# Kernel optimization log

Hardware: AMD Instinct MI355X
Metric: run time of the kernel (lower is better)

## Reference

```python
import jax, jax.numpy as jnp
import numpy as np

EPS = 1e-6
NEG = -10000.0  # matches _merge_attn_masks neg_inf

def rms(x, w):
    return x * jax.lax.rsqrt(jnp.mean(x * x, axis=-1, keepdims=True) + EPS) * w

def setup_inputs() -> dict:
    key = jax.random.key(0)
    ks = jax.random.split(key, 16)
    B, Tq, Tk, D, H, G, dh, F, E = 4, 1024, 1024, 1024, 16, 4, 64, 4096, 8
    s = 1.0 / np.sqrt(D)
    sf = 1.0 / np.sqrt(F)
    return {
        "x": jax.random.normal(ks[0], (B, Tq, D), jnp.float32),
        "k_ctx": jax.random.normal(ks[1], (B, Tk, G, dh), jnp.float32),
        "v_ctx": jax.random.normal(ks[2], (B, Tk, G, dh), jnp.float32),
        "sa_norm_w": jnp.ones((D,), jnp.float32),
        "w_qkv": jax.random.normal(ks[3], (D, 3 * D), jnp.float32) * s,
        "sa_wout": jax.random.normal(ks[4], (D, D), jnp.float32) * s,
        "ca_norm_w": jnp.ones((D,), jnp.float32),
        "w_q": jax.random.normal(ks[5], (D, D), jnp.float32) * s,
        "ca_wout": jax.random.normal(ks[6], (D, D), jnp.float32) * s,
        "moe_norm_w": jnp.ones((D,), jnp.float32),
        "w_gate": jax.random.normal(ks[7], (D, E), jnp.float32) * s,
        "w1": jax.random.normal(ks[8], (E, D, F), jnp.float32) * s,
        "b1": jnp.zeros((E, F), jnp.float32),
        "w2": jax.random.normal(ks[9], (E, F, D), jnp.float32) * sf,
        "b2": jnp.zeros((E, D), jnp.float32),
    }

def _attn(q, k, v, mask=None):
    # q,k,v: [B,H,T,dh]
    dh = q.shape[-1]
    scores = jnp.einsum("bhqd,bhkd->bhqk", q, k) / jnp.sqrt(jnp.float32(dh))
    if mask is not None:
        scores = scores + mask
    p = jax.nn.softmax(scores, axis=-1)
    return jnp.einsum("bhqk,bhkd->bhqd", p, v)

def reference(x, k_ctx, v_ctx, sa_norm_w, w_qkv, sa_wout, ca_norm_w, w_q, ca_wout,
              moe_norm_w, w_gate, w1, b1, w2, b2):
    B, Tq, D = x.shape
    Tk, G, dh = k_ctx.shape[1], k_ctx.shape[2], k_ctx.shape[3]
    H = 16
    rep = H // G

    # ---- self-attention (causal, pre-norm RMS, residual) ----
    xn = rms(x, sa_norm_w)
    qkv = xn @ w_qkv  # [B,Tq,3D]
    q, k, v = jnp.split(qkv, 3, axis=-1)
    split = lambda t: t.reshape(B, Tq, H, dh).transpose(0, 2, 1, 3)
    i = jnp.arange(Tq)[:, None]
    j = jnp.arange(Tq)[None, :]
    causal = jnp.where(j <= i, 0.0, NEG).astype(jnp.float32)[None, None]
    y = _attn(split(q), split(k), split(v), causal)
    y = y.transpose(0, 2, 1, 3).reshape(B, Tq, D) @ sa_wout
    x = x + y

    # ---- cross-attention GQA ----
    qc = rms(x, ca_norm_w) @ w_q
    qc = qc.reshape(B, Tq, H, dh).transpose(0, 2, 1, 3)
    kk = jnp.repeat(k_ctx, rep, axis=2).transpose(0, 2, 1, 3)  # [B,H,Tk,dh]
    vv = jnp.repeat(v_ctx, rep, axis=2).transpose(0, 2, 1, 3)
    yc = _attn(qc, kk, vv)
    yc = yc.transpose(0, 2, 1, 3).reshape(B, Tq, D) @ ca_wout
    x = x + yc

    # ---- top-1 MoE FFN ----
    xm = rms(x, moe_norm_w)
    gate_scores = jax.nn.softmax(xm @ w_gate, axis=-1)  # [B,T,E]
    top1_idx = jnp.argmax(gate_scores, axis=-1)
    top1_score = jnp.max(gate_scores, axis=-1)
    E = w1.shape[0]
    out = jnp.zeros_like(xm)
    for e in range(E):  # small fixed expert count
        ye = jax.nn.silu(xm @ w1[e] + b1[e]) @ w2[e] + b2[e]
        out = jnp.where((top1_idx == e)[..., None], ye, out)
    out = out * top1_score[..., None]
    return x + out
```

## Files before the change

### kernel.cpp

```cpp
#include <hip/hip_runtime.h>
#include <hip/hip_bf16.h>
#include <stdint.h>

#define B_  4
#define T_  1024
#define D_  1024
#define H_  16
#define DH  64
#define F_  4096
#define E_  8
#define NT  (B_*T_)

typedef float f32x4 __attribute__((ext_vector_type(4)));
typedef short bf16x8 __attribute__((ext_vector_type(8)));
#define MFMA_BF16 __builtin_amdgcn_mfma_f32_16x16x32_bf16

union PK8 { uint32_t u[4]; bf16x8 v; };

#define GL16(gsrc, ldst)                                                      \
  __builtin_amdgcn_global_load_lds(                                           \
      (const __attribute__((address_space(1))) void*)(const void*)(gsrc),     \
      (__attribute__((address_space(3))) void*)(void*)(ldst), 16, 0, 0)

static __device__ __forceinline__ uint16_t f2bf(float f) {
  uint32_t u = __float_as_uint(f);
  u += 0x7FFFu + ((u >> 16) & 1u);
  return (uint16_t)(u >> 16);
}
static __device__ __forceinline__ uint32_t packsplit(float f) {
  uint16_t h = f2bf(f);
  float hf = __uint_as_float(((uint32_t)h) << 16);
  uint16_t l = f2bf(f - hf);
  return ((uint32_t)h << 16) | (uint32_t)l;
}
static __device__ __forceinline__ void unpack8(const uint4 p0, const uint4 p1, bf16x8 &hi, bf16x8 &lo) {
  PK8 H, L;
  H.u[0] = __builtin_amdgcn_perm(p0.y, p0.x, 0x07060302u);
  L.u[0] = __builtin_amdgcn_perm(p0.y, p0.x, 0x05040100u);
  H.u[1] = __builtin_amdgcn_perm(p0.w, p0.z, 0x07060302u);
  L.u[1] = __builtin_amdgcn_perm(p0.w, p0.z, 0x05040100u);
  H.u[2] = __builtin_amdgcn_perm(p1.y, p1.x, 0x07060302u);
  L.u[2] = __builtin_amdgcn_perm(p1.y, p1.x, 0x05040100u);
  H.u[3] = __builtin_amdgcn_perm(p1.w, p1.z, 0x07060302u);
  L.u[3] = __builtin_amdgcn_perm(p1.w, p1.z, 0x05040100u);
  hi = H.v; lo = L.v;
}

__global__ __launch_bounds__(256) void k_pack_t2(const float* __restrict__ in,
                                                 uint16_t* __restrict__ outh, uint16_t* __restrict__ outl,
                                                 int K, int N) {
  __shared__ float t[32][33];
  const size_t mo = (size_t)blockIdx.z * K * N;
  in += mo; outh += mo; outl += mo;
  int n0 = blockIdx.x * 32, k0 = blockIdx.y * 32;
  int tx = threadIdx.x & 31, ty = threadIdx.x >> 5;
#pragma unroll
  for (int i = 0; i < 32; i += 8) t[ty + i][tx] = in[(size_t)(k0 + ty + i) * N + n0 + tx];
  __syncthreads();
#pragma unroll
  for (int i = 0; i < 32; i += 8) {
    float v = t[tx][ty + i];
    uint16_t h = f2bf(v);
    uint16_t l = f2bf(v - __uint_as_float((uint32_t)h << 16));
    size_t o = (size_t)(n0 + ty + i) * K + k0 + tx;
    outh[o] = h; outl[o] = l;
  }
}

__global__ __launch_bounds__(256) void k_bf_t(const float* __restrict__ in, uint16_t* __restrict__ out,
                                              int K, int N) {
  __shared__ float t[64][65];
  const size_t mo = (size_t)blockIdx.z * K * N;
  in += mo; out += mo;
  int n0 = blockIdx.x * 64, k0 = blockIdx.y * 64;
  int tr = threadIdx.x >> 4;
  int tc = (threadIdx.x & 15) * 4;
#pragma unroll
  for (int i = 0; i < 64; i += 16) {
    float4 v = *(const float4*)&in[(size_t)(k0 + tr + i) * N + n0 + tc];
    t[tr + i][tc] = v.x; t[tr + i][tc + 1] = v.y; t[tr + i][tc + 2] = v.z; t[tr + i][tc + 3] = v.w;
  }
  __syncthreads();
#pragma unroll
  for (int i = 0; i < 64; i += 16) {
    int n = tr + i;
    uint16_t b0 = f2bf(t[tc][n]), b1 = f2bf(t[tc + 1][n]);
    uint16_t b2 = f2bf(t[tc + 2][n]), b3 = f2bf(t[tc + 3][n]);
    uint2 wv;
    wv.x = ((uint32_t)b1 << 16) | b0;
    wv.y = ((uint32_t)b3 << 16) | b2;
    *(uint2*)&out[(size_t)(n0 + n) * K + k0 + tc] = wv;
  }
}

__global__ __launch_bounds__(256) void k_t32(const uint32_t* __restrict__ in, uint32_t* __restrict__ outp) {
  __shared__ uint32_t t[32][33];
  int b = blockIdx.z, t0 = blockIdx.x * 32, c0 = blockIdx.y * 32;
  int tx = threadIdx.x & 31, ty = threadIdx.x >> 5;
#pragma unroll
  for (int i = 0; i < 32; i += 8)
    t[ty + i][tx] = in[(size_t)(b * T_ + t0 + ty + i) * 3072 + 2048 + c0 + tx];
  __syncthreads();
#pragma unroll
  for (int i = 0; i < 32; i += 8)
    outp[(size_t)(b * T_ + c0 + ty + i) * T_ + t0 + tx] = t[tx][ty + i];
}

__global__ __launch_bounds__(256) void k_packf(const float* __restrict__ in, uint32_t* __restrict__ out) {
  int i = (blockIdx.x * 256 + threadIdx.x) * 4;
  float4 v = *(const float4*)&in[i];
  out[i] = packsplit(v.x); out[i+1] = packsplit(v.y); out[i+2] = packsplit(v.z); out[i+3] = packsplit(v.w);
}

__global__ __launch_bounds__(256) void k_tf32(const float* __restrict__ in, uint32_t* __restrict__ outp) {
  __shared__ float t[32][33];
  int b = blockIdx.z, t0 = blockIdx.x * 32, c0 = blockIdx.y * 32;
  int tx = threadIdx.x & 31, ty = threadIdx.x >> 5;
#pragma unroll
  for (int i = 0; i < 32; i += 8)
    t[ty + i][tx] = in[(size_t)(b * T_ + t0 + ty + i) * 256 + c0 + tx];
  __syncthreads();
#pragma unroll
  for (int i = 0; i < 32; i += 8)
    outp[(size_t)(b * 256 + c0 + ty + i) * T_ + t0 + tx] = packsplit(t[tx][ty + i]);
}

__global__ __launch_bounds__(256) void k_rms(const float* __restrict__ x, const float* __restrict__ w,
                                             uint16_t* __restrict__ oh, uint16_t* __restrict__ ol,
                                             const float* __restrict__ wg, int* __restrict__ idxp,
                                             float* __restrict__ scb) {
  int row = blockIdx.x;
  const float* xr = x + (size_t)row * D_;
  int t = threadIdx.x;
  float4 xv = *(const float4*)&xr[t * 4];
  float s = xv.x * xv.x + xv.y * xv.y + xv.z * xv.z + xv.w * xv.w;
#pragma unroll
  for (int o = 32; o; o >>= 1) s += __shfl_xor(s, o, 64);
  __shared__ float ps[4];
  __shared__ float ga[4][8];
  if ((t & 63) == 0) ps[t >> 6] = s;
  __syncthreads();
  s = ps[0] + ps[1] + ps[2] + ps[3];
  float sc = 1.0f / sqrtf(s * (1.0f / (float)D_) + 1e-6f);
  float4 wv = *(const float4*)&w[t * 4];
  float o0 = xv.x * sc * wv.x, o1 = xv.y * sc * wv.y, o2 = xv.z * sc * wv.z, o3 = xv.w * sc * wv.w;
  uint16_t h0 = f2bf(o0), h1 = f2bf(o1), h2 = f2bf(o2), h3 = f2bf(o3);
  if (oh) {
    uint2 ph;
    ph.x = ((uint32_t)h1 << 16) | h0;
    ph.y = ((uint32_t)h3 << 16) | h2;
    *(uint2*)&oh[(size_t)row * D_ + t * 4] = ph;
  }
  if (ol) {
    uint16_t l0 = f2bf(o0 - __uint_as_float((uint32_t)h0 << 16));
    uint16_t l1 = f2bf(o1 - __uint_as_float((uint32_t)h1 << 16));
    uint16_t l2 = f2bf(o2 - __uint_as_float((uint32_t)h2 << 16));
    uint16_t l3 = f2bf(o3 - __uint_as_float((uint32_t)h3 << 16));
    uint2 pl;
    pl.x = ((uint32_t)l1 << 16) | l0;
    pl.y = ((uint32_t)l3 << 16) | l2;
    *(uint2*)&ol[(size_t)row * D_ + t * 4] = pl;
  }
  if (wg) {
    float a[8] = {};
    float ov[4] = {o0, o1, o2, o3};
#pragma unroll
    for (int j = 0; j < 4; j++) {
      const float* wr = &wg[(size_t)(t * 4 + j) * 8];
      float4 wa = *(const float4*)wr, wb = *(const float4*)(wr + 4);
      float v = ov[j];
      a[0] += v * wa.x; a[1] += v * wa.y; a[2] += v * wa.z; a[3] += v * wa.w;
      a[4] += v * wb.x; a[5] += v * wb.y; a[6] += v * wb.z; a[7] += v * wb.w;
    }
#pragma unroll
    for (int e = 0; e < 8; e++)
#pragma unroll
      for (int o = 32; o; o >>= 1) a[e] += __shfl_xor(a[e], o, 64);
    if ((t & 63) == 0)
#pragma unroll
      for (int e = 0; e < 8; e++) ga[t >> 6][e] = a[e];
    __syncthreads();
    if (t == 0) {
      float g[8];
#pragma unroll
      for (int e = 0; e < 8; e++) g[e] = ga[0][e] + ga[1][e] + ga[2][e] + ga[3][e];
      int bi = 0; float bv = g[0];
#pragma unroll
      for (int e = 1; e < 8; e++) if (g[e] > bv) { bv = g[e]; bi = e; }
      float se = 0.f;
#pragma unroll
      for (int e = 0; e < 8; e++) se += expf(g[e] - bv);
      idxp[row] = bi;
      scb[row] = 1.0f / se;
    }
  }
}

#define GBM 128
#define GBN 64
__global__ __launch_bounds__(256) void k_gemm_split(const uint16_t* __restrict__ Ahg, const uint16_t* __restrict__ Alg,
                                                    const uint16_t* __restrict__ Whg, const uint16_t* __restrict__ Wlg,
                                                    float* __restrict__ C, const float* __restrict__ res,
                                                    uint32_t* __restrict__ Cpk, int scale_cols,
                                                    int M, int N, int K) {
  __shared__ uint16_t Ah[2][GBM][32], Al[2][GBM][32];
  __shared__ uint16_t Wh[2][GBN][32], Wl[2][GBN][32];
  int m0 = blockIdx.y * GBM, n0 = blockIdx.x * GBN;
  int tid = threadIdx.x, wv = tid >> 6, ln = tid & 63, mi = ln & 15, b8 = ln >> 4;
  int lr = ln >> 2, lc = ln & 3;
  int cg = lc ^ (lr & 3);
  int rowA = wv * 32 + lr;
  int rowW = wv * 16 + lr;
  const uint16_t* pAh  = Ahg + (size_t)(m0 + rowA) * K + cg * 8;
  const uint16_t* pAl  = Alg + (size_t)(m0 + rowA) * K + cg * 8;
  const uint16_t* pAh2 = pAh + (size_t)16 * K;
  const uint16_t* pAl2 = pAl + (size_t)16 * K;
  const uint16_t* pWh  = Whg + (size_t)(n0 + rowW) * K + cg * 8;
  const uint16_t* pWl  = Wlg + (size_t)(n0 + rowW) * K + cg * 8;
  const int ch8 = (b8 ^ (mi & 3)) * 8;
  f32x4 acc[2][4] = {};

#define STAGE(bf) do {                                                         \
    GL16(pAh,  &Ah[bf][wv * 32][0]);                                           \
    GL16(pAh2, &Ah[bf][wv * 32 + 16][0]);                                      \
    GL16(pAl,  &Al[bf][wv * 32][0]);                                           \
    GL16(pAl2, &Al[bf][wv * 32 + 16][0]);                                      \
    GL16(pWh,  &Wh[bf][wv * 16][0]);                                           \
    GL16(pWl,  &Wl[bf][wv * 16][0]);                                           \
    pAh += 32; pAh2 += 32; pAl += 32; pAl2 += 32; pWh += 32; pWl += 32;        \
  } while (0)

  const int NK = K >> 5;
  STAGE(0);
  __syncthreads();
  int cur = 0;
  for (int t = 0; t < NK; ++t) {
    if (t + 1 < NK) STAGE(cur ^ 1);
    bf16x8 ah[2], al[2], bh[4], bl[4];
#pragma unroll
    for (int fm = 0; fm < 2; fm++) {
      ah[fm] = *(const bf16x8*)&Ah[cur][wv * 32 + fm * 16 + mi][ch8];
      al[fm] = *(const bf16x8*)&Al[cur][wv * 32 + fm * 16 + mi][ch8];
    }
#pragma unroll
    for (int fn = 0; fn < 4; fn++) {
      bh[fn] = *(const bf16x8*)&Wh[cur][fn * 16 + mi][ch8];
      bl[fn] = *(const bf16x8*)&Wl[cur][fn * 16 + mi][ch8];
    }
#pragma unroll
    for (int fm = 0; fm < 2; fm++)
#pragma unroll
      for (int fn = 0; fn < 4; fn++) {
        acc[fm][fn] = MFMA_BF16(al[fm], bh[fn], acc[fm][fn], 0, 0, 0);
        acc[fm][fn] = MFMA_BF16(ah[fm], bl[fn], acc[fm][fn], 0, 0, 0);
        acc[fm][fn] = MFMA_BF16(ah[fm], bh[fn], acc[fm][fn], 0, 0, 0);
      }
    __syncthreads();
    cur ^= 1;
  }
#undef STAGE
#pragma unroll
  for (int fm = 0; fm < 2; fm++)
#pragma unroll
    for (int fn = 0; fn < 4; fn++)
#pragma unroll
      for (int rr = 0; rr < 4; rr++) {
        int row = m0 + wv * 32 + fm * 16 + b8 * 4 + rr;
        int col = n0 + fn * 16 + mi;
        float v = acc[fm][fn][rr];
        if (Cpk) {
          if (col < scale_cols) v *= 0.125f;
          Cpk[(size_t)row * N + col] = packsplit(v);
        } else {
          if (res) v += res[(size_t)row * N + col];
          C[(size_t)row * N + col] = v;
        }
      }
}

template <bool CAUSAL>
__global__ __launch_bounds__(256, 3) void k_fattn(
    const uint32_t* __restrict__ qp, int qs,
    const uint32_t* __restrict__ kp, int ks_, int khdiv,
    const uint32_t* __restrict__ vtp, int nvrows,
    uint16_t* __restrict__ yhg, uint16_t* __restrict__ ylg) {
  __shared__ uint32_t Ks[64][68];
  __shared__ uint32_t Vs[64][68];
  __shared__ uint32_t Ps[4][32][36];
  const int qt = blockIdx.x, h = blockIdx.y, b = blockIdx.z;
  const int tid = threadIdx.x, wv = tid >> 6, ln = tid & 63, mi = ln & 15, b8 = ln >> 4;
  const int koff = (h / khdiv) * 64;
  const uint32_t* kbase = kp + (size_t)b * T_ * ks_ + koff;
  const uint32_t* vbase = vtp + ((size_t)b * nvrows + koff) * T_;

  bf16x8 qh[2][2], ql[2][2];
#pragma unroll
  for (int u = 0; u < 2; u++)
#pragma unroll
    for (int k2 = 0; k2 < 2; k2++) {
      const uint32_t* p = qp + (size_t)(b * T_ + qt * 128 + wv * 32 + u * 16 + mi) * qs + h * 64 + k2 * 32 + b8 * 8;
      unpack8(*(const uint4*)p, *(const uint4*)(p + 4), qh[u][k2], ql[u][k2]);
    }

  float m[2][4], l[2][4];
  f32x4 o[2][4] = {};
#pragma unroll
  for (int u = 0; u < 2; u++)
#pragma unroll
    for (int r = 0; r < 4; r++) { m[u][r] = -1e30f; l[u][r] = 0.f; }

  const int nkt = CAUSAL ? (2 * qt + 2) : (T_ / 64);
  for (int kt = 0; kt < nkt; kt++) {
    __syncthreads();
    {
      int rr = tid >> 2, cc = (tid & 3) * 16;
      const uint32_t* src = kbase + (size_t)(kt * 64 + rr) * ks_ + cc;
      *(uint4*)&Ks[rr][cc]      = *(const uint4*)src;
      *(uint4*)&Ks[rr][cc + 4]  = *(const uint4*)(src + 4);
      *(uint4*)&Ks[rr][cc + 8]  = *(const uint4*)(src + 8);
      *(uint4*)&Ks[rr][cc + 12] = *(const uint4*)(src + 12);
      const uint32_t* vsrc = vbase + (size_t)rr * T_ + kt * 64 + cc;
      *(uint4*)&Vs[rr][cc]      = *(const uint4*)vsrc;
      *(uint4*)&Vs[rr][cc + 4]  = *(const uint4*)(vsrc + 4);
      *(uint4*)&Vs[rr][cc + 8]  = *(const uint4*)(vsrc + 8);
      *(uint4*)&Vs[rr][cc + 12] = *(const uint4*)(vsrc + 12);
    }
    __syncthreads();
#pragma unroll
    for (int s = 0; s < 2; s++) {
      bf16x8 kh[2][2], kl[2][2];
#pragma unroll
      for (int nf = 0; nf < 2; nf++)
#pragma unroll
        for (int k2 = 0; k2 < 2; k2++) {
          const uint32_t* p = &Ks[s * 32 + nf * 16 + mi][k2 * 32 + b8 * 8];
          unpack8(*(const uint4*)p, *(const uint4*)(p + 4), kh[nf][k2], kl[nf][k2]);
        }
      f32x4 a[2][2] = {};
#pragma unroll
      for (int u = 0; u < 2; u++)
#pragma unroll
        for (int nf = 0; nf < 2; nf++)
#pragma unroll
          for (int k2 = 0; k2 < 2; k2++) {
            a[u][nf] = MFMA_BF16(ql[u][k2], kh[nf][k2], a[u][nf], 0, 0, 0);
            a[u][nf] = MFMA_BF16(qh[u][k2], kl[nf][k2], a[u][nf], 0, 0, 0);
            a[u][nf] = MFMA_BF16(qh[u][k2], kh[nf][k2], a[u][nf], 0, 0, 0);
          }
      if (CAUSAL && kt >= 2 * qt) {
        int kg = kt * 64 + s * 32 + mi;
#pragma unroll
        for (int u = 0; u < 2; u++) {
          int qg = qt * 128 + wv * 32 + u * 16 + b8 * 4;
#pragma unroll
          for (int r = 0; r < 4; r++) {
            if (kg > qg + r)      a[u][0][r] = -1e30f;
            if (kg + 16 > qg + r) a[u][1][r] = -1e30f;
          }
        }
      }
#pragma unroll
      for (int u = 0; u < 2; u++) {
        float pm[4];
#pragma unroll
        for (int r = 0; r < 4; r++) pm[r] = fmaxf(a[u][0][r], a[u][1][r]);
#pragma unroll
        for (int off = 1; off <= 8; off <<= 1)
#pragma unroll
          for (int r = 0; r < 4; r++) pm[r] = fmaxf(pm[r], __shfl_xor(pm[r], off, 64));
        float sc[4];
#pragma unroll
        for (int r = 0; r < 4; r++) {
          float mn = fmaxf(m[u][r], pm[r]);
          sc[r] = __expf(m[u][r] - mn);
          m[u][r] = mn;
          a[u][0][r] = __expf(a[u][0][r] - mn);
          a[u][1][r] = __expf(a[u][1][r] - mn);
        }
        float rs[4];
#pragma unroll
        for (int r = 0; r < 4; r++) rs[r] = a[u][0][r] + a[u][1][r];
#pragma unroll
        for (int off = 1; off <= 8; off <<= 1)
#pragma unroll
          for (int r = 0; r < 4; r++) rs[r] += __shfl_xor(rs[r], off, 64);
#pragma unroll
        for (int r = 0; r < 4; r++) l[u][r] = l[u][r] * sc[r] + rs[r];
#pragma unroll
        for (int f = 0; f < 4; f++)
#pragma unroll
          for (int r = 0; r < 4; r++) o[u][f][r] *= sc[r];
#pragma unroll
        for (int r = 0; r < 4; r++) {
          uint32_t Hw, Lw;
          asm("v_cvt_pk_bf16_f32 %0, %1, %2" : "=v"(Hw) : "v"(a[u][0][r]), "v"(a[u][1][r]));
          float h0 = __uint_as_float(Hw << 16);
          float h1 = __uint_as_float(Hw & 0xffff0000u);
          float r0 = a[u][0][r] - h0, r1 = a[u][1][r] - h1;
          asm("v_cvt_pk_bf16_f32 %0, %1, %2" : "=v"(Lw) : "v"(r0), "v"(r1));
          Ps[wv][u * 16 + b8 * 4 + r][mi]      = __builtin_amdgcn_perm(Hw, Lw, 0x05040100u);
          Ps[wv][u * 16 + b8 * 4 + r][16 + mi] = __builtin_amdgcn_perm(Hw, Lw, 0x07060302u);
        }
      }
      bf16x8 ph[2], pl[2];
#pragma unroll
      for (int u = 0; u < 2; u++) {
        const uint32_t* p = &Ps[wv][u * 16 + mi][b8 * 8];
        unpack8(*(const uint4*)p, *(const uint4*)(p + 4), ph[u], pl[u]);
      }
#pragma unroll
      for (int f = 0; f < 4; f++) {
        bf16x8 vh, vl;
        const uint32_t* p = &Vs[f * 16 + mi][s * 32 + b8 * 8];
        unpack8(*(const uint4*)p, *(const uint4*)(p + 4), vh, vl);
#pragma unroll
        for (int u = 0; u < 2; u++) {
          o[u][f] = MFMA_BF16(pl[u], vh, o[u][f], 0, 0, 0);
          o[u][f] = MFMA_BF16(ph[u], vl, o[u][f], 0, 0, 0);
          o[u][f] = MFMA_BF16(ph[u], vh, o[u][f], 0, 0, 0);
        }
      }
    }
  }
#pragma unroll
  for (int u = 0; u < 2; u++)
#pragma unroll
    for (int r = 0; r < 4; r++) {
      float inv = 1.0f / l[u][r];
      int row = qt * 128 + wv * 32 + u * 16 + b8 * 4 + r;
#pragma unroll
      for (int f = 0; f < 4; f++) {
        size_t idx = (size_t)(b * T_ + row) * D_ + h * 64 + f * 16 + mi;
        float v = o[u][f][r] * inv;
        uint16_t hv = f2bf(v);
        yhg[idx] = hv;
        ylg[idx] = f2bf(v - __uint_as_float((uint32_t)hv << 16));
      }
    }
}

__global__ __launch_bounds__(256) void k_bucket(const int* __restrict__ idx, int* __restrict__ cnt,
                                                int* __restrict__ lists) {
  int tok = blockIdx.x * 256 + threadIdx.x;
  int e = idx[tok];
  int p = atomicAdd(&cnt[e], 1);
  lists[e * NT + p] = tok;
}

__global__ __launch_bounds__(256) void k_moe1(const uint16_t* __restrict__ xmbf, const uint16_t* __restrict__ w1t,
                                              const float* __restrict__ b1, const int* __restrict__ cnt,
                                              const int* __restrict__ lists, uint16_t* __restrict__ hbf) {
  int e = blockIdx.z;
  int c = cnt[e];
  int m0 = blockIdx.y * 64;
  if (m0 >= c) return;
  int n0 = blockIdx.x * 64;
  __shared__ uint16_t As[64][72];
  __shared__ uint16_t Ws[64][72];
  __shared__ int toks[64];
  int tid = threadIdx.x, wv = tid >> 6, ln = tid & 63, mi = ln & 15, b8 = ln >> 4;
  if (tid < 64) toks[tid] = (m0 + tid < c) ? lists[e * NT + m0 + tid] : -1;
  __syncthreads();
  int r = tid >> 2, c16 = (tid & 3) * 16;
  int tk = toks[r];
  const uint16_t* asrc = (tk >= 0) ? (xmbf + (size_t)tk * D_ + c16) : nullptr;
  const uint16_t* wsrc = w1t + (size_t)e * F_ * D_ + (size_t)(n0 + r) * D_ + c16;
  f32x4 acc[4] = {};
  for (int k0 = 0; k0 < D_; k0 += 64) {
    {
      uint4 a0 = make_uint4(0, 0, 0, 0), a1 = make_uint4(0, 0, 0, 0);
      if (asrc) { a0 = *(const uint4*)(asrc + k0); a1 = *(const uint4*)(asrc + k0 + 8); }
      uint4 w0 = *(const uint4*)(wsrc + k0), w1v = *(const uint4*)(wsrc + k0 + 8);
      *(uint4*)&As[r][c16] = a0; *(uint4*)&As[r][c16 + 8] = a1;
      *(uint4*)&Ws[r][c16] = w0; *(uint4*)&Ws[r][c16 + 8] = w1v;
    }
    __syncthreads();
#pragma unroll
    for (int ks = 0; ks < 2; ks++) {
      bf16x8 a = *(const bf16x8*)&As[wv * 16 + mi][ks * 32 + b8 * 8];
#pragma unroll
      for (int fn = 0; fn < 4; fn++) {
        bf16x8 bb = *(const bf16x8*)&Ws[fn * 16 + mi][ks * 32 + b8 * 8];
        acc[fn] = MFMA_BF16(a, bb, acc[fn], 0, 0, 0);
      }
    }
    __syncthreads();
  }
#pragma unroll
  for (int fn = 0; fn < 4; fn++)
#pragma unroll
    for (int rr = 0; rr < 4; rr++) {
      int rt = wv * 16 + b8 * 4 + rr;
      if (m0 + rt < c) {
        int tok = toks[rt];
        int col = n0 + fn * 16 + mi;
        float v = acc[fn][rr] + b1[e * F_ + col];
        v = v / (1.0f + expf(-v));
        hbf[(size_t)tok * F_ + col] = f2bf(v);
      }
    }
}

__global__ __launch_bounds__(256) void k_moe2(const uint16_t* __restrict__ hbf, const uint16_t* __restrict__ w2t,
                                              const float* __restrict__ b2, const float* __restrict__ x2,
                                              const float* __restrict__ sc, const int* __restrict__ cnt,
                                              const int* __restrict__ lists, float* __restrict__ out) {
  int e = blockIdx.z;
  int c = cnt[e];
  int m0 = blockIdx.y * 64;
  if (m0 >= c) return;
  int n0 = blockIdx.x * 64;
  __shared__ uint16_t As[64][72];
  __shared__ uint16_t Ws[64][72];
  __shared__ int toks[64];
  int tid = threadIdx.x, wv = tid >> 6, ln = tid & 63, mi = ln & 15, b8 = ln >> 4;
  if (tid < 64) toks[tid] = (m0 + tid < c) ? lists[e * NT + m0 + tid] : -1;
  __syncthreads();
  int r = tid >> 2, c16 = (tid & 3) * 16;
  int tk = toks[r];
  const uint16_t* asrc = (tk >= 0) ? (hbf + (size_t)tk * F_ + c16) : nullptr;
  const uint16_t* wsrc = w2t + (size_t)e * D_ * F_ + (size_t)(n0 + r) * F_ + c16;
  f32x4 acc[4] = {};
  for (int k0 = 0; k0 < F_; k0 += 64) {
    {
      uint4 a0 = make_uint4(0, 0, 0, 0), a1 = make_uint4(0, 0, 0, 0);
      if (asrc) { a0 = *(const uint4*)(asrc + k0); a1 = *(const uint4*)(asrc + k0 + 8); }
      uint4 w0 = *(const uint4*)(wsrc + k0), w1v = *(const uint4*)(wsrc + k0 + 8);
      *(uint4*)&As[r][c16] = a0; *(uint4*)&As[r][c16 + 8] = a1;
      *(uint4*)&Ws[r][c16] = w0; *(uint4*)&Ws[r][c16 + 8] = w1v;
    }
    __syncthreads();
#pragma unroll
    for (int ks = 0; ks < 2; ks++) {
      bf16x8 a = *(const bf16x8*)&As[wv * 16 + mi][ks * 32 + b8 * 8];
#pragma unroll
      for (int fn = 0; fn < 4; fn++) {
        bf16x8 bb = *(const bf16x8*)&Ws[fn * 16 + mi][ks * 32 + b8 * 8];
        acc[fn] = MFMA_BF16(a, bb, acc[fn], 0, 0, 0);
      }
    }
    __syncthreads();
  }
#pragma unroll
  for (int fn = 0; fn < 4; fn++)
#pragma unroll
    for (int rr = 0; rr < 4; rr++) {
      int rt = wv * 16 + b8 * 4 + rr;
      if (m0 + rt < c) {
        int tok = toks[rt];
        int col = n0 + fn * 16 + mi;
        float v = acc[fn][rr] + b2[e * D_ + col];
        out[(size_t)tok * D_ + col] = x2[(size_t)tok * D_ + col] + sc[tok] * v;
      }
    }
}

extern "C" void kernel_launch(void* const* d_in, const int* in_sizes, int n_in,
                              void* d_out, int out_size, void* d_ws, size_t ws_size,
                              hipStream_t stream) {
  const float* x       = (const float*)d_in[0];
  const float* k_ctx   = (const float*)d_in[1];
  const float* v_ctx   = (const float*)d_in[2];
  const float* sa_nw   = (const float*)d_in[3];
  const float* w_qkv   = (const float*)d_in[4];
  const float* sa_wout = (const float*)d_in[5];
  const float* ca_nw   = (const float*)d_in[6];
  const float* w_q     = (const float*)d_in[7];
  const float* ca_wout = (const float*)d_in[8];
  const float* moe_nw  = (const float*)d_in[9];
  const float* w_gate  = (const float*)d_in[10];
  const float* w1      = (const float*)d_in[11];
  const float* b1      = (const float*)d_in[12];
  const float* w2      = (const float*)d_in[13];
  const float* b2      = (const float*)d_in[14];
  float* out = (float*)d_out;
  (void)in_sizes; (void)n_in; (void)out_size; (void)ws_size;

  char* ws = (char*)d_ws;
  size_t off = 0;
  auto alloc = [&](size_t bytes) { char* p = ws + off; off += (bytes + 255) & ~(size_t)255; return p; };
  uint16_t* xnh   = (uint16_t*)alloc((size_t)NT * D_ * 2);
  uint16_t* xnl   = (uint16_t*)alloc((size_t)NT * D_ * 2);
  uint16_t* yh    = (uint16_t*)alloc((size_t)NT * D_ * 2);
  uint16_t* yl    = (uint16_t*)alloc((size_t)NT * D_ * 2);
  float*    x1    = (float*)alloc((size_t)NT * D_ * 4);
  uint32_t* qkv_pk = (uint32_t*)alloc((size_t)NT * 3 * D_ * 4);
  uint32_t* qc_pk = qkv_pk;
  float* x2 = (float*)(qkv_pk + (size_t)NT * D_);
  uint16_t* wqkvTh = (uint16_t*)alloc((size_t)D_ * 3 * D_ * 2);
  uint16_t* wqkvTl = (uint16_t*)alloc((size_t)D_ * 3 * D_ * 2);
  uint16_t* sawTh  = (uint16_t*)alloc((size_t)D_ * D_ * 2);
  uint16_t* sawTl  = (uint16_t*)alloc((size_t)D_ * D_ * 2);
  uint16_t* wqTh   = (uint16_t*)alloc((size_t)D_ * D_ * 2);
  uint16_t* wqTl   = (uint16_t*)alloc((size_t)D_ * D_ * 2);
  uint16_t* cawTh  = (uint16_t*)alloc((size_t)D_ * D_ * 2);
  uint16_t* cawTl  = (uint16_t*)alloc((size_t)D_ * D_ * 2);
  uint16_t* w1t   = (uint16_t*)alloc((size_t)E_ * D_ * F_ * 2);
  uint16_t* w2t   = (uint16_t*)alloc((size_t)E_ * D_ * F_ * 2);
  uint16_t* hbf   = (uint16_t*)alloc((size_t)NT * F_ * 2);
  uint32_t* vt    = (uint32_t*)hbf;
  uint32_t* kc_pk = (uint32_t*)((char*)hbf + (size_t)16 * 1024 * 1024);
  uint32_t* vct   = (uint32_t*)((char*)hbf + (size_t)20 * 1024 * 1024);
  uint16_t* xmbf  = (uint16_t*)alloc((size_t)NT * D_ * 2);
  int*   idx   = (int*)alloc(NT * 4);
  float* scb   = (float*)alloc(NT * 4);
  int*   cnt   = (int*)alloc(256);
  int*   lists = (int*)alloc((size_t)E_ * NT * 4);

  k_pack_t2<<<dim3(3 * D_ / 32, D_ / 32, 1), 256, 0, stream>>>(w_qkv, wqkvTh, wqkvTl, D_, 3 * D_);
  k_pack_t2<<<dim3(D_ / 32, D_ / 32, 1), 256, 0, stream>>>(sa_wout, sawTh, sawTl, D_, D_);
  k_pack_t2<<<dim3(D_ / 32, D_ / 32, 1), 256, 0, stream>>>(w_q, wqTh, wqTl, D_, D_);
  k_pack_t2<<<dim3(D_ / 32, D_ / 32, 1), 256, 0, stream>>>(ca_wout, cawTh, cawTl, D_, D_);
  k_bf_t<<<dim3(F_ / 64, D_ / 64, E_), 256, 0, stream>>>(w1, w1t, D_, F_);
  k_bf_t<<<dim3(D_ / 64, F_ / 64, E_), 256, 0, stream>>>(w2, w2t, F_, D_);
  k_packf<<<(B_ * T_ * 256) / 1024, 256, 0, stream>>>(k_ctx, kc_pk);
  k_tf32<<<dim3(T_ / 32, 256 / 32, B_), 256, 0, stream>>>(v_ctx, vct);

  k_rms<<<NT, 256, 0, stream>>>(x, sa_nw, xnh, xnl, nullptr, nullptr, nullptr);
  k_gemm_split<<<dim3(3 * D_ / GBN, NT / GBM), 256, 0, stream>>>(xnh, xnl, wqkvTh, wqkvTl, nullptr, nullptr, qkv_pk, 1024, NT, 3 * D_, D_);
  k_t32<<<dim3(T_ / 32, D_ / 32, B_), 256, 0, stream>>>(qkv_pk, vt);
  k_fattn<true><<<dim3(T_ / 128, H_, B_), 256, 0, stream>>>(qkv_pk, 3072, qkv_pk + 1024, 3072, 1, vt, 1024, yh, yl);
  k_gemm_split<<<dim3(D_ / GBN, NT / GBM), 256, 0, stream>>>(yh, yl, sawTh, sawTl, x1, x, nullptr, 0, NT, D_, D_);

  k_rms<<<NT, 256, 0, stream>>>(x1, ca_nw, xnh, xnl, nullptr, nullptr, nullptr);
  k_gemm_split<<<dim3(D_ / GBN, NT / GBM), 256, 0, stream>>>(xnh, xnl, wqTh, wqTl, nullptr, nullptr, qc_pk, 1024, NT, D_, D_);
  k_fattn<false><<<dim3(T_ / 128, H_, B_), 256, 0, stream>>>(qc_pk, 1024, kc_pk, 256, 4, vct, 256, yh, yl);
  k_gemm_split<<<dim3(D_ / GBN, NT / GBM), 256, 0, stream>>>(yh, yl, cawTh, cawTl, x2, x1, nullptr, 0, NT, D_, D_);

  k_rms<<<NT, 256, 0, stream>>>(x2, moe_nw, xmbf, nullptr, w_gate, idx, scb);
  hipMemsetAsync(cnt, 0, 32, stream);
  k_bucket<<<NT / 256, 256, 0, stream>>>(idx, cnt, lists);
  k_moe1<<<dim3(F_ / 64, NT / 64, E_), 256, 0, stream>>>(xmbf, w1t, b1, cnt, lists, hbf);
  k_moe2<<<dim3(D_ / 64, NT / 64, E_), 256, 0, stream>>>(hbf, w2t, b2, x2, scb, cnt, lists, out);
}
```

Before: 852.4 us.

## Store attention operands as separate bf16 hi/lo planes instead of packed words

```diff
diff --git a/kernel.cpp b/kernel.cpp
--- a/kernel.cpp
+++ b/kernel.cpp
@@ -26,12 +26,6 @@
   uint32_t u = __float_as_uint(f);
   u += 0x7FFFu + ((u >> 16) & 1u);
   return (uint16_t)(u >> 16);
-}
-static __device__ __forceinline__ uint32_t packsplit(float f) {
-  uint16_t h = f2bf(f);
-  float hf = __uint_as_float(((uint32_t)h) << 16);
-  uint16_t l = f2bf(f - hf);
-  return ((uint32_t)h << 16) | (uint32_t)l;
 }
 static __device__ __forceinline__ void unpack8(const uint4 p0, const uint4 p1, bf16x8 &hi, bf16x8 &lo) {
   PK8 H, L;
@@ -93,26 +87,51 @@
   }
 }
 
-__global__ __launch_bounds__(256) void k_t32(const uint32_t* __restrict__ in, uint32_t* __restrict__ outp) {
-  __shared__ uint32_t t[32][33];
-  int b = blockIdx.z, t0 = blockIdx.x * 32, c0 = blockIdx.y * 32;
-  int tx = threadIdx.x & 31, ty = threadIdx.x >> 5;
-#pragma unroll
-  for (int i = 0; i < 32; i += 8)
-    t[ty + i][tx] = in[(size_t)(b * T_ + t0 + ty + i) * 3072 + 2048 + c0 + tx];
-  __syncthreads();
-#pragma unroll
-  for (int i = 0; i < 32; i += 8)
-    outp[(size_t)(b * T_ + c0 + ty + i) * T_ + t0 + tx] = t[tx][ty + i];
-}
-
-__global__ __launch_bounds__(256) void k_packf(const float* __restrict__ in, uint32_t* __restrict__ out) {
+__global__ __launch_bounds__(256) void k_t16(const uint16_t* __restrict__ inh, const uint16_t* __restrict__ inl,
+                                             uint16_t* __restrict__ outh, uint16_t* __restrict__ outl) {
+  __shared__ uint16_t th[64][68], tl[64][68];
+  int b = blockIdx.z, t0 = blockIdx.x * 64, c0 = blockIdx.y * 64;
+  int tr = threadIdx.x >> 4;
+  int tc = (threadIdx.x & 15) * 4;
+#pragma unroll
+  for (int i = 0; i < 64; i += 16) {
+    size_t src = (size_t)(b * T_ + t0 + tr + i) * 3072 + 2048 + c0 + tc;
+    *(uint2*)&th[tr + i][tc] = *(const uint2*)&inh[src];
+    *(uint2*)&tl[tr + i][tc] = *(const uint2*)&inl[src];
+  }
+  __syncthreads();
+#pragma unroll
+  for (int i = 0; i < 64; i += 16) {
+    int n = tr + i;
+    size_t dst = (size_t)(b * 1024 + c0 + n) * T_ + t0 + tc;
+    uint2 ph, pl;
+    ph.x = ((uint32_t)th[tc + 1][n] << 16) | th[tc][n];
+    ph.y = ((uint32_t)th[tc + 3][n] << 16) | th[tc + 2][n];
+    pl.x = ((uint32_t)tl[tc + 1][n] << 16) | tl[tc][n];
+    pl.y = ((uint32_t)tl[tc + 3][n] << 16) | tl[tc + 2][n];
+    *(uint2*)&outh[dst] = ph;
+    *(uint2*)&outl[dst] = pl;
+  }
+}
+
+__global__ __launch_bounds__(256) void k_packf2(const float* __restrict__ in,
+                                                uint16_t* __restrict__ oh, uint16_t* __restrict__ ol) {
   int i = (blockIdx.x * 256 + threadIdx.x) * 4;
   float4 v = *(const float4*)&in[i];
-  out[i] = packsplit(v.x); out[i+1] = packsplit(v.y); out[i+2] = packsplit(v.z); out[i+3] = packsplit(v.w);
-}
-
-__global__ __launch_bounds__(256) void k_tf32(const float* __restrict__ in, uint32_t* __restrict__ outp) {
+  uint16_t h0 = f2bf(v.x), h1 = f2bf(v.y), h2 = f2bf(v.z), h3 = f2bf(v.w);
+  uint2 ph, pl;
+  ph.x = ((uint32_t)h1 << 16) | h0;
+  ph.y = ((uint32_t)h3 << 16) | h2;
+  pl.x = ((uint32_t)f2bf(v.y - __uint_as_float((uint32_t)h1 << 16)) << 16) |
+         f2bf(v.x - __uint_as_float((uint32_t)h0 << 16));
+  pl.y = ((uint32_t)f2bf(v.w - __uint_as_float((uint32_t)h3 << 16)) << 16) |
+         f2bf(v.z - __uint_as_float((uint32_t)h2 << 16));
+  *(uint2*)&oh[i] = ph;
+  *(uint2*)&ol[i] = pl;
+}
+
+__global__ __launch_bounds__(256) void k_tf32(const float* __restrict__ in,
+                                              uint16_t* __restrict__ oh, uint16_t* __restrict__ ol) {
   __shared__ float t[32][33];
   int b = blockIdx.z, t0 = blockIdx.x * 32, c0 = blockIdx.y * 32;
   int tx = threadIdx.x & 31, ty = threadIdx.x >> 5;
@@ -121,8 +140,13 @@
     t[ty + i][tx] = in[(size_t)(b * T_ + t0 + ty + i) * 256 + c0 + tx];
   __syncthreads();
 #pragma unroll
-  for (int i = 0; i < 32; i += 8)
-    outp[(size_t)(b * 256 + c0 + ty + i) * T_ + t0 + tx] = packsplit(t[tx][ty + i]);
+  for (int i = 0; i < 32; i += 8) {
+    float v = t[tx][ty + i];
+    uint16_t h = f2bf(v);
+    size_t o = (size_t)(b * 256 + c0 + ty + i) * T_ + t0 + tx;
+    oh[o] = h;
+    ol[o] = f2bf(v - __uint_as_float((uint32_t)h << 16));
+  }
 }
 
 __global__ __launch_bounds__(256) void k_rms(const float* __restrict__ x, const float* __restrict__ w,
@@ -201,8 +225,8 @@
 __global__ __launch_bounds__(256) void k_gemm_split(const uint16_t* __restrict__ Ahg, const uint16_t* __restrict__ Alg,
                                                     const uint16_t* __restrict__ Whg, const uint16_t* __restrict__ Wlg,
                                                     float* __restrict__ C, const float* __restrict__ res,
-                                                    uint32_t* __restrict__ Cpk, int scale_cols,
-                                                    int M, int N, int K) {
+                                                    uint16_t* __restrict__ Cph, uint16_t* __restrict__ Cpl,
+                                                    int scale_cols, int M, int N, int K) {
   __shared__ uint16_t Ah[2][GBM][32], Al[2][GBM][32];
   __shared__ uint16_t Wh[2][GBN][32], Wl[2][GBN][32];
   int m0 = blockIdx.y * GBM, n0 = blockIdx.x * GBN;
@@ -268,38 +292,45 @@
         int row = m0 + wv * 32 + fm * 16 + b8 * 4 + rr;
         int col = n0 + fn * 16 + mi;
         float v = acc[fm][fn][rr];
-        if (Cpk) {
+        size_t o = (size_t)row * N + col;
+        if (Cph) {
           if (col < scale_cols) v *= 0.125f;
-          Cpk[(size_t)row * N + col] = packsplit(v);
+          uint16_t hv = f2bf(v);
+          Cph[o] = hv;
+          Cpl[o] = f2bf(v - __uint_as_float((uint32_t)hv << 16));
         } else {
-          if (res) v += res[(size_t)row * N + col];
-          C[(size_t)row * N + col] = v;
+          if (res) v += res[o];
+          C[o] = v;
         }
       }
 }
 
 template <bool CAUSAL>
 __global__ __launch_bounds__(256, 3) void k_fattn(
-    const uint32_t* __restrict__ qp, int qs,
-    const uint32_t* __restrict__ kp, int ks_, int khdiv,
-    const uint32_t* __restrict__ vtp, int nvrows,
+    const uint16_t* __restrict__ qhg, const uint16_t* __restrict__ qlg, int qs,
+    const uint16_t* __restrict__ khg, const uint16_t* __restrict__ klg, int ks_, int khdiv,
+    const uint16_t* __restrict__ vhg, const uint16_t* __restrict__ vlg, int nvrows,
     uint16_t* __restrict__ yhg, uint16_t* __restrict__ ylg) {
-  __shared__ uint32_t Ks[64][68];
-  __shared__ uint32_t Vs[64][68];
+  __shared__ uint16_t Ksh[64][68], Ksl[64][68];
+  __shared__ uint16_t Vsh[64][68], Vsl[64][68];
   __shared__ uint32_t Ps[4][32][36];
-  const int qt = blockIdx.x, h = blockIdx.y, b = blockIdx.z;
+  const int h = blockIdx.y, b = blockIdx.z;
+  const int qt = CAUSAL ? ((blockIdx.x + h + 2 * b) & 7) : blockIdx.x;
   const int tid = threadIdx.x, wv = tid >> 6, ln = tid & 63, mi = ln & 15, b8 = ln >> 4;
   const int koff = (h / khdiv) * 64;
-  const uint32_t* kbase = kp + (size_t)b * T_ * ks_ + koff;
-  const uint32_t* vbase = vtp + ((size_t)b * nvrows + koff) * T_;
+  const uint16_t* kbh = khg + (size_t)b * T_ * ks_ + koff;
+  const uint16_t* kbl = klg + (size_t)b * T_ * ks_ + koff;
+  const uint16_t* vbh = vhg + ((size_t)b * nvrows + koff) * T_;
+  const uint16_t* vbl = vlg + ((size_t)b * nvrows + koff) * T_;
 
   bf16x8 qh[2][2], ql[2][2];
 #pragma unroll
   for (int u = 0; u < 2; u++)
 #pragma unroll
     for (int k2 = 0; k2 < 2; k2++) {
-      const uint32_t* p = qp + (size_t)(b * T_ + qt * 128 + wv * 32 + u * 16 + mi) * qs + h * 64 + k2 * 32 + b8 * 8;
-      unpack8(*(const uint4*)p, *(const uint4*)(p + 4), qh[u][k2], ql[u][k2]);
+      size_t o = (size_t)(b * T_ + qt * 128 + wv * 32 + u * 16 + mi) * qs + h * 64 + k2 * 32 + b8 * 8;
+      qh[u][k2] = *(const bf16x8*)&qhg[o];
+      ql[u][k2] = *(const bf16x8*)&qlg[o];
     }
 
   float m[2][4], l[2][4];
@@ -314,16 +345,16 @@
     __syncthreads();
     {
       int rr = tid >> 2, cc = (tid & 3) * 16;
-      const uint32_t* src = kbase + (size_t)(kt * 64 + rr) * ks_ + cc;
-      *(uint4*)&Ks[rr][cc]      = *(const uint4*)src;
-      *(uint4*)&Ks[rr][cc + 4]  = *(const uint4*)(src + 4);
-      *(uint4*)&Ks[rr][cc + 8]  = *(const uint4*)(src + 8);
-      *(uint4*)&Ks[rr][cc + 12] = *(const uint4*)(src + 12);
-      const uint32_t* vsrc = vbase + (size_t)rr * T_ + kt * 64 + cc;
-      *(uint4*)&Vs[rr][cc]      = *(const uint4*)vsrc;
-      *(uint4*)&Vs[rr][cc + 4]  = *(const uint4*)(vsrc + 4);
-      *(uint4*)&Vs[rr][cc + 8]  = *(const uint4*)(vsrc + 8);
-      *(uint4*)&Vs[rr][cc + 12] = *(const uint4*)(vsrc + 12);
+      size_t ko = (size_t)(kt * 64 + rr) * ks_ + cc;
+      *(uint4*)&Ksh[rr][cc]     = *(const uint4*)&kbh[ko];
+      *(uint4*)&Ksh[rr][cc + 8] = *(const uint4*)&kbh[ko + 8];
+      *(uint4*)&Ksl[rr][cc]     = *(const uint4*)&kbl[ko];
+      *(uint4*)&Ksl[rr][cc + 8] = *(const uint4*)&kbl[ko + 8];
+      size_t vo = (size_t)rr * T_ + kt * 64 + cc;
+      *(uint4*)&Vsh[rr][cc]     = *(const uint4*)&vbh[vo];
+      *(uint4*)&Vsh[rr][cc + 8] = *(const uint4*)&vbh[vo + 8];
+      *(uint4*)&Vsl[rr][cc]     = *(const uint4*)&vbl[vo];
+      *(uint4*)&Vsl[rr][cc + 8] = *(const uint4*)&vbl[vo + 8];
     }
     __syncthreads();
 #pragma unroll
@@ -333,8 +364,9 @@
       for (int nf = 0; nf < 2; nf++)
 #pragma unroll
         for (int k2 = 0; k2 < 2; k2++) {
-          const uint32_t* p = &Ks[s * 32 + nf * 16 + mi][k2 * 32 + b8 * 8];
-          unpack8(*(const uint4*)p, *(const uint4*)(p + 4), kh[nf][k2], kl[nf][k2]);
+          int rrow = s * 32 + nf * 16 + mi, ccol = k2 * 32 + b8 * 8;
+          kh[nf][k2] = *(const bf16x8*)&Ksh[rrow][ccol];
+          kl[nf][k2] = *(const bf16x8*)&Ksl[rrow][ccol];
         }
       f32x4 a[2][2] = {};
 #pragma unroll
@@ -410,9 +442,9 @@
       }
 #pragma unroll
       for (int f = 0; f < 4; f++) {
-        bf16x8 vh, vl;
-        const uint32_t* p = &Vs[f * 16 + mi][s * 32 + b8 * 8];
-        unpack8(*(const uint4*)p, *(const uint4*)(p + 4), vh, vl);
+        int rrow = f * 16 + mi, ccol = s * 32 + b8 * 8;
+        bf16x8 vh = *(const bf16x8*)&Vsh[rrow][ccol];
+        bf16x8 vl = *(const bf16x8*)&Vsl[rrow][ccol];
 #pragma unroll
         for (int u = 0; u < 2; u++) {
           o[u][f] = MFMA_BF16(pl[u], vh, o[u][f], 0, 0, 0);
@@ -584,9 +616,11 @@
   uint16_t* yh    = (uint16_t*)alloc((size_t)NT * D_ * 2);
   uint16_t* yl    = (uint16_t*)alloc((size_t)NT * D_ * 2);
   float*    x1    = (float*)alloc((size_t)NT * D_ * 4);
-  uint32_t* qkv_pk = (uint32_t*)alloc((size_t)NT * 3 * D_ * 4);
-  uint32_t* qc_pk = qkv_pk;
-  float* x2 = (float*)(qkv_pk + (size_t)NT * D_);
+  uint16_t* qkvh  = (uint16_t*)alloc((size_t)NT * 3 * D_ * 2);
+  uint16_t* qkvl  = (uint16_t*)alloc((size_t)NT * 3 * D_ * 2);
+  float* x2 = (float*)qkvh;
+  uint16_t* qch = qkvl;
+  uint16_t* qcl = qkvl + (size_t)NT * D_;
   uint16_t* wqkvTh = (uint16_t*)alloc((size_t)D_ * 3 * D_ * 2);
   uint16_t* wqkvTl = (uint16_t*)alloc((size_t)D_ * 3 * D_ * 2);
   uint16_t* sawTh  = (uint16_t*)alloc((size_t)D_ * D_ * 2);
@@ -598,9 +632,12 @@
   uint16_t* w1t   = (uint16_t*)alloc((size_t)E_ * D_ * F_ * 2);
   uint16_t* w2t   = (uint16_t*)alloc((size_t)E_ * D_ * F_ * 2);
   uint16_t* hbf   = (uint16_t*)alloc((size_t)NT * F_ * 2);
-  uint32_t* vt    = (uint32_t*)hbf;
-  uint32_t* kc_pk = (uint32_t*)((char*)hbf + (size_t)16 * 1024 * 1024);
-  uint32_t* vct   = (uint32_t*)((char*)hbf + (size_t)20 * 1024 * 1024);
+  uint16_t* vth   = (uint16_t*)hbf;
+  uint16_t* vtl   = vth + (size_t)NT * D_;
+  uint16_t* kch   = (uint16_t*)((char*)hbf + (size_t)16 * 1024 * 1024);
+  uint16_t* kcl   = (uint16_t*)((char*)hbf + (size_t)18 * 1024 * 1024);
+  uint16_t* vcth  = (uint16_t*)((char*)hbf + (size_t)20 * 1024 * 1024);
+  uint16_t* vctl  = (uint16_t*)((char*)hbf + (size_t)22 * 1024 * 1024);
   uint16_t* xmbf  = (uint16_t*)alloc((size_t)NT * D_ * 2);
   int*   idx   = (int*)alloc(NT * 4);
   float* scb   = (float*)alloc(NT * 4);
@@ -613,19 +650,19 @@
   k_pack_t2<<<dim3(D_ / 32, D_ / 32, 1), 256, 0, stream>>>(ca_wout, cawTh, cawTl, D_, D_);
   k_bf_t<<<dim3(F_ / 64, D_ / 64, E_), 256, 0, stream>>>(w1, w1t, D_, F_);
   k_bf_t<<<dim3(D_ / 64, F_ / 64, E_), 256, 0, stream>>>(w2, w2t, F_, D_);
-  k_packf<<<(B_ * T_ * 256) / 1024, 256, 0, stream>>>(k_ctx, kc_pk);
-  k_tf32<<<dim3(T_ / 32, 256 / 32, B_), 256, 0, stream>>>(v_ctx, vct);
+  k_packf2<<<(B_ * T_ * 256) / 1024, 256, 0, stream>>>(k_ctx, kch, kcl);
+  k_tf32<<<dim3(T_ / 32, 256 / 32, B_), 256, 0, stream>>>(v_ctx, vcth, vctl);
 
   k_rms<<<NT, 256, 0, stream>>>(x, sa_nw, xnh, xnl, nullptr, nullptr, nullptr);
-  k_gemm_split<<<dim3(3 * D_ / GBN, NT / GBM), 256, 0, stream>>>(xnh, xnl, wqkvTh, wqkvTl, nullptr, nullptr, qkv_pk, 1024, NT, 3 * D_, D_);
-  k_t32<<<dim3(T_ / 32, D_ / 32, B_), 256, 0, stream>>>(qkv_pk, vt);
-  k_fattn<true><<<dim3(T_ / 128, H_, B_), 256, 0, stream>>>(qkv_pk, 3072, qkv_pk + 1024, 3072, 1, vt, 1024, yh, yl);
-  k_gemm_split<<<dim3(D_ / GBN, NT / GBM), 256, 0, stream>>>(yh, yl, sawTh, sawTl, x1, x, nullptr, 0, NT, D_, D_);
+  k_gemm_split<<<dim3(3 * D_ / GBN, NT / GBM), 256, 0, stream>>>(xnh, xnl, wqkvTh, wqkvTl, nullptr, nullptr, qkvh, qkvl, 1024, NT, 3 * D_, D_);
+  k_t16<<<dim3(T_ / 64, D_ / 64, B_), 256, 0, stream>>>(qkvh, qkvl, vth, vtl);
+  k_fattn<true><<<dim3(T_ / 128, H_, B_), 256, 0, stream>>>(qkvh, qkvl, 3072, qkvh + 1024, qkvl + 1024, 3072, 1, vth, vtl, 1024, yh, yl);
+  k_gemm_split<<<dim3(D_ / GBN, NT / GBM), 256, 0, stream>>>(yh, yl, sawTh, sawTl, x1, x, nullptr, nullptr, 0, NT, D_, D_);
 
   k_rms<<<NT, 256, 0, stream>>>(x1, ca_nw, xnh, xnl, nullptr, nullptr, nullptr);
-  k_gemm_split<<<dim3(D_ / GBN, NT / GBM), 256, 0, stream>>>(xnh, xnl, wqTh, wqTl, nullptr, nullptr, qc_pk, 1024, NT, D_, D_);
-  k_fattn<false><<<dim3(T_ / 128, H_, B_), 256, 0, stream>>>(qc_pk, 1024, kc_pk, 256, 4, vct, 256, yh, yl);
-  k_gemm_split<<<dim3(D_ / GBN, NT / GBM), 256, 0, stream>>>(yh, yl, cawTh, cawTl, x2, x1, nullptr, 0, NT, D_, D_);
+  k_gemm_split<<<dim3(D_ / GBN, NT / GBM), 256, 0, stream>>>(xnh, xnl, wqTh, wqTl, nullptr, nullptr, qch, qcl, 1024, NT, D_, D_);
+  k_fattn<false><<<dim3(T_ / 128, H_, B_), 256, 0, stream>>>(qch, qcl, 1024, kch, kcl, 256, 4, vcth, vctl, 256, yh, yl);
+  k_gemm_split<<<dim3(D_ / GBN, NT / GBM), 256, 0, stream>>>(yh, yl, cawTh, cawTl, x2, x1, nullptr, nullptr, 0, NT, D_, D_);
 
   k_rms<<<NT, 256, 0, stream>>>(x2, moe_nw, xmbf, nullptr, w_gate, idx, scb);
   hipMemsetAsync(cnt, 0, 32, stream);
```

After: 845.4 us. No clear change (-0.8%).
